# Optimization experiments

Hardware: AMD Instinct MI355X
Metric: run time of the kernel (lower is better)

## Reference

```python
import jax, jax.numpy as jnp
import numpy as np
from jax import lax

IN_CH = 64
OUT_CH = 64
K = 3
CW = 2 * IN_CH + 49  # in_ch_weight = 2*in_ch + MAX_DISPLACEMENT**2 = 177
B = 8


def setup_inputs() -> dict:
    key = jax.random.key(0)
    ks = jax.random.split(key, 14)
    f = lambda k, s, sc: jax.random.normal(k, s, dtype=jnp.float32) * sc
    he5 = lambda cin: (2.0 / (cin * 25)) ** 0.5
    he3 = lambda cin: (2.0 / (cin * 9)) ** 0.5
    return {
        "x0": f(ks[0], (B, IN_CH, 128, 160), 1.0),
        "y0": f(ks[1], (B, IN_CH, 128, 160), 1.0),
        "x": f(ks[2], (B, IN_CH, 64, 80), 1.0),
        "y": f(ks[3], (B, IN_CH, 64, 80), 1.0),
        # weight-branch 0 (outputs CW channels)
        "w1a": f(ks[4], (IN_CH, CW, 5, 5), he5(CW)),
        "w1b": f(ks[5], (IN_CH, IN_CH, 5, 5), he5(IN_CH)),
        "w1c": f(ks[6], (CW, IN_CH, 3, 3), he3(IN_CH)),
        # weight-branch 1 / final (outputs OUT_CH channels)
        "w2a": f(ks[7], (IN_CH, CW, 5, 5), he5(CW)),
        "w2b": f(ks[8], (IN_CH, IN_CH, 5, 5), he5(IN_CH)),
        "w2c": f(ks[9], (OUT_CH, IN_CH, 3, 3), he3(IN_CH)),
        # grouped 1x1 dynamic-weight generators (per-channel affine maps)
        "wx_w": f(ks[10], (CW, CW * K * K), 0.05),
        "wx_b": f(ks[11], (CW, CW * K * K), 0.05),
        "wxf_w": f(ks[12], (OUT_CH, OUT_CH * K * K), 0.05),
        "wxf_b": f(ks[13], (OUT_CH, OUT_CH * K * K), 0.05),
    }


def _conv(x, w, stride, pad):
    return lax.conv_general_dilated(
        x, w, (stride, stride), [(pad, pad), (pad, pad)],
        dimension_numbers=("NCHW", "OIHW", "NCHW"))


def _pool2(x):
    b, c, h, w = x.shape
    return x.reshape(b, c, h // 2, 2, w // 2, 2).mean(axis=(3, 5))


def _corr(x0, y0):
    # FlowNet-style correlation: max_displacement=7, stride2=2 ->
    # displacements {-6,-4,-2,0,2,4,6}^2 = 49 channels; mean over C.
    b, c, h, w = x0.shape
    D = 6
    yp = jnp.pad(y0, ((0, 0), (0, 0), (D, D), (D, D)))
    outs = []
    for dy in range(-6, 7, 2):
        for dx in range(-6, 7, 2):
            ys = yp[:, :, D + dy:D + dy + h, D + dx:D + dx + w]
            outs.append(jnp.mean(x0 * ys, axis=1))
    return jnp.stack(outs, axis=1)  # [B, 49, H, W]


def _branch(feat, wa, wb, wc):
    h = jax.nn.relu(_conv(feat, wa, 2, 2))
    h = jax.nn.relu(_conv(h, wb, 2, 2))
    h = _conv(h, wc, 2, 1)
    return h.mean(axis=(2, 3))  # adaptive_avg_pool2d -> (1,1), squeezed: [B, Cout]


def _adaptive_conv(x, w, pad):
    # per-sample conv weights w: [B, Cout, Cin, k, k]
    def one(xb, wb):
        return _conv(xb[None], wb, 1, pad)[0]
    return jax.vmap(one)(x, w)


def reference(x0, y0, x, y, w1a, w1b, w1c, w2a, w2b, w2c, wx_w, wx_b, wxf_w, wxf_b):
    b = x.shape[0]
    x0p = _pool2(x0)
    y0p = _pool2(y0)
    corr = _corr(x0p, y0p)                      # [B, 49, H, W]
    feat = jnp.concatenate([corr, x, y], axis=1)  # [B, CW, H, W]

    # iteration 0 (N-1 = 1): generate per-sample [CW,CW,3,3] filters, apply
    fv = _branch(feat, w1a, w1b, w1c)           # [B, CW]
    wx = (fv[:, :, None] * wx_w[None] + wx_b[None]).reshape(b, CW, CW, K, K)
    feat = jax.nn.relu(_adaptive_conv(feat, wx, K // 2))

    # final: generate per-sample [OUT_CH,OUT_CH,3,3] filters and return them
    fv = _branch(feat, w2a, w2b, w2c)           # [B, OUT_CH]
    wxf = (fv[:, :, None] * wxf_w[None] + wxf_b[None]).reshape(b, OUT_CH, OUT_CH, K, K)
    return wxf
```

## Files before the change

kernel.cpp:

```cpp
#include <hip/hip_runtime.h>

typedef unsigned short u16;
typedef __attribute__((ext_vector_type(8))) short bf16x8;
typedef __attribute__((ext_vector_type(4))) float f32x4;

static constexpr int B  = 8;
static constexpr int C  = 64;
static constexpr int CW = 177;
static constexpr int H  = 64, W  = 80;
static constexpr int HP = 68, WP = 84, KC = 192;
static constexpr int PB = HP * WP * KC;
static constexpr int HA = 36, WA = 44;

__device__ __forceinline__ u16 f2b(float f) {
  union { float f; unsigned u; } v; v.f = f;
  unsigned u = v.u;
  return (u16)((u + 0x7FFF + ((u >> 16) & 1)) >> 16);
}
__device__ __forceinline__ float blo(unsigned u) {
  union { unsigned v; float f; } t; t.v = u << 16; return t.f;
}
__device__ __forceinline__ float bhi(unsigned u) {
  union { unsigned v; float f; } t; t.v = u & 0xffff0000u; return t.f;
}
__device__ __forceinline__ unsigned pk2(u16 a, u16 b) {
  return (unsigned)a | ((unsigned)b << 16);
}

__global__ void zfill2(u16* __restrict__ p1, int n1, u16* __restrict__ p2, int n2) {
  int i = blockIdx.x * blockDim.x + threadIdx.x;
  bf16x8 z = 0;
  if (i < n1) ((bf16x8*)p1)[i] = z;
  else if (i < n1 + n2) ((bf16x8*)p2)[i - n1] = z;
}

__global__ __launch_bounds__(256) void pool2_kernel(const float* __restrict__ x0, const float* __restrict__ y0,
                                                    u16* __restrict__ xpT, u16* __restrict__ ypT) {
  __shared__ u16 lt[80][66];
  int blk = blockIdx.x;
  int sel = blk & 1; int h = (blk >> 1) & 63; int b = blk >> 7;
  const float* in = sel ? y0 : x0;
  u16* out = sel ? ypT : xpT;
  int tid = threadIdx.x;
#pragma unroll
  for (int i = 0; i < 20; ++i) {
    int e = i * 256 + tid;
    int c = e / 80, w = e % 80;
    const float* p = in + ((size_t)(b * 64 + c) * 128 + 2 * h) * 160 + 2 * w;
    float2 r0 = *(const float2*)p;
    float2 r1 = *(const float2*)(p + 160);
    lt[w][c] = f2b(0.25f * (r0.x + r0.y + r1.x + r1.y));
  }
  __syncthreads();
#pragma unroll
  for (int i = 0; i < 20; ++i) {
    int e = i * 256 + tid;
    int w = e / 64, c = e % 64;
    out[((size_t)(b * H + h) * W + w) * C + c] = lt[w][c];
  }
}

__global__ void corr_fill(const u16* __restrict__ xpT, const u16* __restrict__ ypT,
                          u16* __restrict__ featP) {
  int idx = blockIdx.x * blockDim.x + threadIdx.x;
  if (idx >= B * H * W * 49) return;
  int o = idx % 49; int p = idx / 49;
  int w = p % W; int h = (p / W) % H; int b = p / (W * H);
  int dy = (o / 7) * 2 - 6, dx = (o % 7) * 2 - 6;
  int hh = h + dy, ww = w + dx;
  float s = 0.f;
  if (hh >= 0 && hh < H && ww >= 0 && ww < W) {
    const uint4* xv = (const uint4*)(xpT + ((size_t)(b * H + h) * W + w) * C);
    const uint4* yv = (const uint4*)(ypT + ((size_t)(b * H + hh) * W + ww) * C);
#pragma unroll
    for (int i = 0; i < 8; ++i) {
      uint4 a = xv[i], q = yv[i];
      s += blo(a.x) * blo(q.x) + bhi(a.x) * bhi(q.x);
      s += blo(a.y) * blo(q.y) + bhi(a.y) * bhi(q.y);
      s += blo(a.z) * blo(q.z) + bhi(a.z) * bhi(q.z);
      s += blo(a.w) * blo(q.w) + bhi(a.w) * bhi(q.w);
    }
  }
  s *= (1.0f / 64.0f);
  featP[((size_t)(b * HP + h + 2) * WP + (w + 2)) * KC + o] = f2b(s);
}

__global__ __launch_bounds__(256) void copy_tr(const float* __restrict__ x, const float* __restrict__ y,
                                               u16* __restrict__ featP) {
  __shared__ float lt[40][129];
  int blk = blockIdx.x;
  int half = blk & 1; int h = (blk >> 1) & 63; int b = blk >> 7;
  int tid = threadIdx.x;
#pragma unroll
  for (int i = 0; i < 20; ++i) {
    int e = i * 256 + tid;
    int c2 = e / 40, w = e % 40;
    const float* src = (c2 < 64) ? x : y;
    int c = c2 & 63;
    lt[w][c2] = src[((size_t)(b * 64 + c) * H + h) * W + half * 40 + w];
  }
  __syncthreads();
#pragma unroll
  for (int i = 0; i < 20; ++i) {
    int e = i * 256 + tid;
    int wr = e / 128, c = e % 128;
    featP[((size_t)(b * HP + h + 2) * WP + (half * 40 + wr + 2)) * KC + 49 + c] = f2b(lt[wr][c]);
  }
}

__global__ void pack_all(const float* __restrict__ w1a, const float* __restrict__ w2a,
                         const float* __restrict__ w1b, const float* __restrict__ w2b,
                         u16* __restrict__ A5a, u16* __restrict__ A5b,
                         u16* __restrict__ A5b1, u16* __restrict__ A5b2) {
  int idx = blockIdx.x * blockDim.x + threadIdx.x;
  const int s1 = 25 * 64 * 192, s2 = 25 * 64 * 64;
  if (idx < 2 * s1) {
    const float* w = idx < s1 ? w1a : w2a; u16* A = idx < s1 ? A5a : A5b;
    int e = idx % s1;
    int j = e % 192; int i = (e / 192) % 64; int kk = e / (192 * 64);
    int ky = kk / 5, kx = kk % 5;
    float v = (j < CW) ? w[(((size_t)i * CW + j) * 5 + ky) * 5 + kx] : 0.f;
    A[e] = f2b(v);
  } else if (idx < 2 * s1 + 2 * s2) {
    int t = idx - 2 * s1;
    const float* w = t < s2 ? w1b : w2b; u16* A = t < s2 ? A5b1 : A5b2;
    int e = t % s2;
    int j = e % 64; int i = (e / 64) % 64; int kk = e / (64 * 64);
    int ky = kk / 5, kx = kk % 5;
    A[e] = f2b(w[(((size_t)i * 64 + j) * 5 + ky) * 5 + kx]);
  }
}

__global__ void halo_fill(u16* __restrict__ featP) {
  int idx = blockIdx.x * blockDim.x + threadIdx.x;
  if (idx >= B * 592 * 24) return;
  int ch = idx % 24; int pi = (idx / 24) % 592; int b = idx / (24 * 592);
  int row, col;
  if (pi < 336) {
    int r = pi / 84; row = (r < 2) ? r : r + 64; col = pi % 84;
  } else {
    int pj = pi - 336; row = 2 + (pj >> 2);
    int cc = pj & 3; col = (cc < 2) ? cc : cc + 80;
  }
  bf16x8 z = 0;
  *(bf16x8*)(featP + ((size_t)(b * HP + row) * WP + col) * KC + ch * 8) = z;
}

__global__ void wx_pack(const float* __restrict__ fv, const float* __restrict__ ww,
                        const float* __restrict__ wb, u16* __restrict__ Apk) {
  int idx = blockIdx.x * blockDim.x + threadIdx.x;
  if (idx >= 9 * 192 * 24) return;
  int j8 = idx % 24; int i = (idx / 24) % 192; int kk = idx / (24 * 192);
  float wwv[8], wbv[8];
#pragma unroll
  for (int jj = 0; jj < 8; ++jj) {
    int j = j8 * 8 + jj;
    if (i < CW && j < CW) {
      size_t o = ((size_t)i * CW + j) * 9 + kk;
      wwv[jj] = ww[o]; wbv[jj] = wb[o];
    } else { wwv[jj] = 0.f; wbv[jj] = 0.f; }
  }
  int rb = i >> 4, il = i & 15;
  int c = j8 >> 3, rem = j8 & 7, half = rem >> 2, kqq = rem & 3;
  size_t dst = (((((size_t)kk * 12 + rb) * 3 + c) * 2 + half) * 64 + kqq * 16 + il) * 8;
  for (int b = 0; b < B; ++b) {
    float f = (i < CW) ? fv[b * CW + i] : 0.f;
    u16 o[8];
#pragma unroll
    for (int jj = 0; jj < 8; ++jj) o[jj] = f2b(f * wwv[jj] + wbv[jj]);
    uint4 v; v.x = pk2(o[0], o[1]); v.y = pk2(o[2], o[3]); v.z = pk2(o[4], o[5]); v.w = pk2(o[6], o[7]);
    *(uint4*)(Apk + (size_t)b * 331776 + dst) = v;
  }
}

__global__ __launch_bounds__(256, 2) void ad_conv_kernel(
    const u16* __restrict__ Apk, const u16* __restrict__ featP, u16* __restrict__ outP) {
  __shared__ u16 lds[2][84 * 64];
  int bid = (int)(blockIdx.x % 8) * 64 + (int)(blockIdx.x / 8);
  int h = bid & 63; int b = bid >> 6;
  int tid = threadIdx.x;
  int lane = tid & 63; int wm = tid >> 6;
  int l15 = lane & 15, kq = lane >> 4;

  f32x4 acc[3][5];
#pragma unroll
  for (int i = 0; i < 3; ++i)
#pragma unroll
    for (int j = 0; j < 5; ++j) acc[i][j] = (f32x4){0.f, 0.f, 0.f, 0.f};

  const u16* fb = featP + (size_t)b * PB;
  const u16* Ab = Apk + (size_t)b * 331776 + (size_t)lane * 8;

  int i0 = tid, i1 = tid + 256, i2 = tid + 512;
  int q0 = i0 >> 3, s0 = i0 & 7;
  int q1 = i1 >> 3, s1 = i1 & 7;
  int q2 = i2 >> 3, s2 = i2 & 7;
  int w0 = (i0 * 16) ^ ((q0 & 7) << 4);
  int w1 = (i1 * 16) ^ ((q1 & 7) << 4);
  int w2 = (i2 * 16) ^ ((q2 & 7) << 4);
  bool a2 = i2 < 672;

  bf16x8 r0, r1, r2;
  {
    const u16* g = fb + ((size_t)(h + 1) * WP) * KC;
    r0 = *(const bf16x8*)(g + (size_t)q0 * KC + s0 * 8);
    r1 = *(const bf16x8*)(g + (size_t)q1 * KC + s1 * 8);
    if (a2) r2 = *(const bf16x8*)(g + (size_t)q2 * KC + s2 * 8);
    char* lw = (char*)lds[0];
    *(bf16x8*)(lw + w0) = r0;
    *(bf16x8*)(lw + w1) = r1;
    if (a2) *(bf16x8*)(lw + w2) = r2;
  }
  __syncthreads();

#pragma unroll
  for (int s = 0; s < 9; ++s) {
    const int c = s / 3, ty = s % 3;
    if (s < 8) {
      const int cn = (s + 1) / 3, tyn = (s + 1) % 3;
      const u16* g = fb + ((size_t)(h + 1 + tyn) * WP) * KC + cn * 64;
      r0 = *(const bf16x8*)(g + (size_t)q0 * KC + s0 * 8);
      r1 = *(const bf16x8*)(g + (size_t)q1 * KC + s1 * 8);
      if (a2) r2 = *(const bf16x8*)(g + (size_t)q2 * KC + s2 * 8);
    }
    const char* lb = (const char*)lds[s & 1];
#pragma unroll
    for (int tx = 0; tx < 3; ++tx) {
      const int tap = ty * 3 + tx;
#pragma unroll
      for (int half = 0; half < 2; ++half) {
        bf16x8 av[3], bv[5];
#pragma unroll
        for (int fm = 0; fm < 3; ++fm)
          av[fm] = *(const bf16x8*)(Ab + (size_t)(((tap * 12 + wm * 3 + fm) * 3 + c) * 2 + half) * 512);
#pragma unroll
        for (int fn = 0; fn < 5; ++fn) {
          int q = fn * 16 + l15 + tx + 1;
          int byte = ((q * 8 + half * 4 + kq) * 16) ^ ((q & 7) << 4);
          bv[fn] = *(const bf16x8*)(lb + byte);
        }
#pragma unroll
        for (int fm = 0; fm < 3; ++fm)
#pragma unroll
          for (int fn = 0; fn < 5; ++fn)
            acc[fm][fn] = __builtin_amdgcn_mfma_f32_16x16x32_bf16(av[fm], bv[fn], acc[fm][fn], 0, 0, 0);
      }
    }
    if (s < 8) {
      char* lw = (char*)lds[(s + 1) & 1];
      *(bf16x8*)(lw + w0) = r0;
      *(bf16x8*)(lw + w1) = r1;
      if (a2) *(bf16x8*)(lw + w2) = r2;
      __syncthreads();
    }
  }

#pragma unroll
  for (int fm = 0; fm < 3; ++fm) {
    int i0r = wm * 48 + fm * 16 + kq * 4;
#pragma unroll
    for (int fn = 0; fn < 5; ++fn) {
      int ow = fn * 16 + l15;
      u16* dst = outP + ((size_t)(b * HP + h + 2) * WP + (ow + 2)) * KC + i0r;
      uint2 pkv;
      pkv.x = pk2(f2b(fmaxf(acc[fm][fn][0], 0.f)), f2b(fmaxf(acc[fm][fn][1], 0.f)));
      pkv.y = pk2(f2b(fmaxf(acc[fm][fn][2], 0.f)), f2b(fmaxf(acc[fm][fn][3], 0.f)));
      *(uint2*)dst = pkv;
    }
  }
}

__global__ __launch_bounds__(128, 3) void conv5_split_kernel(
    const u16* __restrict__ A5, const u16* __restrict__ featP, u16* __restrict__ pa) {
  __shared__ u16 lds[2 * 84 * 32];
  char* lb = (char*)lds;
  int bid = (int)(blockIdx.x % 8) * 160 + (int)(blockIdx.x / 8);
  int rp = bid % 16; int ty = (bid / 16) % 5; int csel = (bid / 80) % 2; int b = bid / 160;
  int r0 = rp * 2;
  int kc0 = csel * 3;
  int tid = threadIdx.x;
  int lane = tid & 63; int wm = tid >> 6;
  int l15 = lane & 15, kq = lane >> 4;

  f32x4 acc[2][5];
#pragma unroll
  for (int i = 0; i < 2; ++i)
#pragma unroll
    for (int j = 0; j < 5; ++j) acc[i][j] = (f32x4){0.f, 0.f, 0.f, 0.f};

  const u16* fb = featP + (size_t)b * PB;
  int rowg0 = 2 * r0 + ty;

#pragma unroll
  for (int k = 0; k < 3; ++k) {
    int kc = kc0 + k;
    __syncthreads();
#pragma unroll
    for (int it = 0; it < 6; ++it) {
      int idx = it * 128 + tid;
      if (idx < 672) {
        int slot = idx & 3; int q = (idx >> 2) % 84; int row = idx / 336;
        bf16x8 v = *(const bf16x8*)(fb + ((size_t)(rowg0 + 2 * row) * WP + q) * KC + kc * 32 + slot * 8);
        int byte = (idx * 16) ^ ((q & 7) << 4);
        *(bf16x8*)(lb + byte) = v;
      }
    }
    __syncthreads();
#pragma unroll
    for (int tx = 0; tx < 5; ++tx) {
      bf16x8 av[2], bv[5];
#pragma unroll
      for (int fm = 0; fm < 2; ++fm)
        av[fm] = *(const bf16x8*)(A5 + ((size_t)((ty * 5 + tx) * 64 + wm * 32 + fm * 16 + l15)) * 192 + kc * 32 + kq * 8);
#pragma unroll
      for (int fn = 0; fn < 5; ++fn) {
        int p = fn * 16 + l15;
        int orow = p / 40, ocol = p % 40;
        int q = ocol * 2 + tx;
        int byte = (((orow * 84 + q) * 4 + kq) * 16) ^ ((q & 7) << 4);
        bv[fn] = *(const bf16x8*)(lb + byte);
      }
#pragma unroll
      for (int fm = 0; fm < 2; ++fm)
#pragma unroll
        for (int fn = 0; fn < 5; ++fn)
          acc[fm][fn] = __builtin_amdgcn_mfma_f32_16x16x32_bf16(av[fm], bv[fn], acc[fm][fn], 0, 0, 0);
    }
  }
  int slot10 = csel * 5 + ty;
#pragma unroll
  for (int fm = 0; fm < 2; ++fm) {
    int oc0 = wm * 32 + fm * 16 + kq * 4;
#pragma unroll
    for (int fn = 0; fn < 5; ++fn) {
      int p = fn * 16 + l15;
      int orow = r0 + p / 40, ocol = p % 40;
      u16* dst = pa + (((((size_t)slot10 * B + b) * 32 + orow) * 40 + ocol) * 64) + oc0;
      uint2 pkv;
      pkv.x = pk2(f2b(acc[fm][fn][0]), f2b(acc[fm][fn][1]));
      pkv.y = pk2(f2b(acc[fm][fn][2]), f2b(acc[fm][fn][3]));
      *(uint2*)dst = pkv;
    }
  }
}

__global__ void combine10(const u16* __restrict__ pa, u16* __restrict__ haP) {
  int idx = blockIdx.x * blockDim.x + threadIdx.x;
  if (idx >= B * 32 * 40 * 8) return;
  int c8 = idx & 7; int t = idx >> 3;
  int ocol = t % 40; t /= 40; int orow = t % 32; int b = t / 32;
  float s[8];
#pragma unroll
  for (int k = 0; k < 8; ++k) s[k] = 0.f;
#pragma unroll
  for (int sl = 0; sl < 10; ++sl) {
    const u16* p = pa + ((((size_t)sl * B + b) * 32 + orow) * 40 + ocol) * 64 + c8 * 8;
    uint4 v = *(const uint4*)p;
    s[0] += blo(v.x); s[1] += bhi(v.x); s[2] += blo(v.y); s[3] += bhi(v.y);
    s[4] += blo(v.z); s[5] += bhi(v.z); s[6] += blo(v.w); s[7] += bhi(v.w);
  }
  uint4 o;
  o.x = pk2(f2b(fmaxf(s[0], 0.f)), f2b(fmaxf(s[1], 0.f)));
  o.y = pk2(f2b(fmaxf(s[2], 0.f)), f2b(fmaxf(s[3], 0.f)));
  o.z = pk2(f2b(fmaxf(s[4], 0.f)), f2b(fmaxf(s[5], 0.f)));
  o.w = pk2(f2b(fmaxf(s[6], 0.f)), f2b(fmaxf(s[7], 0.f)));
  *(uint4*)(haP + ((size_t)(b * HA + orow + 2) * WA + (ocol + 2)) * 64 + c8 * 8) = o;
}

template<int TY, int TX, int S, int OH, int OW, int M, int BM, int BN, int POFF,
         int KCIN, int HPIN, int WPIN>
__global__ __launch_bounds__(256) void gemm_conv(
    const u16* __restrict__ A, const u16* __restrict__ featP,
    float* __restrict__ outF, int MT, int NT) {
  constexpr int WM = BM / 2, WN = BN / 2, FM = WM / 16, FN = WN / 16;
  constexpr int NKC = KCIN / 32;
  int nwg = gridDim.x;
  int bid = (int)(blockIdx.x % 8) * (nwg / 8) + (int)(blockIdx.x / 8);
  int mt = bid % MT; int rest = bid / MT; int nt = rest % NT; int b = rest / NT;
  int lane = threadIdx.x & 63; int wv = threadIdx.x >> 6;
  int wm = wv >> 1, wn = wv & 1;
  int l15 = lane & 15, kq = lane >> 4;

  f32x4 acc[FM][FN];
#pragma unroll
  for (int i = 0; i < FM; ++i)
#pragma unroll
    for (int j = 0; j < FN; ++j) acc[i][j] = (f32x4){0.f, 0.f, 0.f, 0.f};

  const u16* Abase = A + (size_t)(mt * BM + wm * WM + l15) * KCIN + kq * 8;
  const u16* fb = featP + (size_t)b * (HPIN * WPIN * KCIN) + kq * 8;

  int ohh[FN], oww[FN];
#pragma unroll
  for (int fn = 0; fn < FN; ++fn) {
    int p = nt * BN + wn * WN + fn * 16 + l15;
    ohh[fn] = p / OW; oww[fn] = p % OW;
  }

  for (int kc = 0; kc < NKC; ++kc) {
    for (int ty = 0; ty < TY; ++ty)
      for (int tx = 0; tx < TX; ++tx) {
        const u16* At = Abase + (size_t)((ty * TX + tx) * M) * KCIN + kc * 32;
        bf16x8 av[FM], bv[FN];
#pragma unroll
        for (int fm = 0; fm < FM; ++fm)
          av[fm] = *(const bf16x8*)(At + fm * 16 * KCIN);
#pragma unroll
        for (int fn = 0; fn < FN; ++fn) {
          int hi = ohh[fn] * S + ty + POFF;
          int wi = oww[fn] * S + tx + POFF;
          bv[fn] = *(const bf16x8*)(fb + (size_t)(hi * WPIN + wi) * KCIN + kc * 32);
        }
#pragma unroll
        for (int fm = 0; fm < FM; ++fm)
#pragma unroll
          for (int fn = 0; fn < FN; ++fn)
            acc[fm][fn] = __builtin_amdgcn_mfma_f32_16x16x32_bf16(av[fm], bv[fn], acc[fm][fn], 0, 0, 0);
      }
  }

#pragma unroll
  for (int fm = 0; fm < FM; ++fm) {
    int oc0 = mt * BM + wm * WM + fm * 16 + kq * 4;
#pragma unroll
    for (int fn = 0; fn < FN; ++fn) {
#pragma unroll
      for (int r = 0; r < 4; ++r) {
        float v = fmaxf(acc[fm][fn][r], 0.f);
        outF[(((size_t)b * M + oc0 + r) * OH + ohh[fn]) * OW + oww[fn]] = v;
      }
    }
  }
}

__global__ void tapsum_kernel(const float* __restrict__ hb, float* __restrict__ Sm) {
  int b = blockIdx.x >> 6; int ic = blockIdx.x & 63; int lane = threadIdx.x;
  const float* p = hb + ((size_t)(b * 64 + ic)) * 320;
  float s[9];
#pragma unroll
  for (int t = 0; t < 9; ++t) s[t] = 0.f;
  for (int i = lane; i < 320; i += 64) {
    int ih = i / 20, iw = i % 20;
    float v = p[i];
#pragma unroll
    for (int ky = 0; ky < 3; ++ky) {
      int t2 = ih + 1 - ky;
      if (t2 < 0 || t2 > 14 || (t2 & 1)) continue;
#pragma unroll
      for (int kx = 0; kx < 3; ++kx) {
        int t3 = iw + 1 - kx;
        if (t3 < 0 || t3 > 18 || (t3 & 1)) continue;
        s[ky * 3 + kx] += v;
      }
    }
  }
#pragma unroll
  for (int t = 0; t < 9; ++t)
#pragma unroll
    for (int off = 32; off > 0; off >>= 1) s[t] += __shfl_down(s[t], off);
  if (lane == 0) {
#pragma unroll
    for (int t = 0; t < 9; ++t) Sm[(b * 64 + ic) * 9 + t] = s[t];
  }
}

__global__ void gemv_fv(const float* __restrict__ w3, const float* __restrict__ Sm,
                        float* __restrict__ fv, int OC) {
  int o = blockIdx.x % OC; int b = blockIdx.x / OC; int lane = threadIdx.x;
  const float* wp = w3 + ((size_t)o * 64 + lane) * 9;
  const float* sp = Sm + ((size_t)b * 64 + lane) * 9;
  float acc = 0.f;
#pragma unroll
  for (int t = 0; t < 9; ++t) acc += wp[t] * sp[t];
#pragma unroll
  for (int off = 32; off > 0; off >>= 1) acc += __shfl_down(acc, off);
  if (lane == 0) fv[b * OC + o] = acc * (1.0f / 80.0f);
}

__global__ void final_kernel(const float* __restrict__ fv, const float* __restrict__ ww,
                             const float* __restrict__ wb, float* __restrict__ out) {
  int idx = blockIdx.x * blockDim.x + threadIdx.x;
  if (idx >= B * 64 * 576) return;
  int kk = idx % 576; int i = (idx / 576) % 64; int b = idx / (576 * 64);
  out[idx] = fv[b * 64 + i] * ww[i * 576 + kk] + wb[i * 576 + kk];
}

extern "C" void kernel_launch(void* const* d_in, const int* in_sizes, int n_in,
                              void* d_out, int out_size, void* d_ws, size_t ws_size,
                              hipStream_t stream) {
  const float* x0    = (const float*)d_in[0];
  const float* y0    = (const float*)d_in[1];
  const float* x     = (const float*)d_in[2];
  const float* y     = (const float*)d_in[3];
  const float* w1a   = (const float*)d_in[4];
  const float* w1b   = (const float*)d_in[5];
  const float* w1c   = (const float*)d_in[6];
  const float* w2a   = (const float*)d_in[7];
  const float* w2b   = (const float*)d_in[8];
  const float* w2c   = (const float*)d_in[9];
  const float* wx_w  = (const float*)d_in[10];
  const float* wx_b  = (const float*)d_in[11];
  const float* wxf_w = (const float*)d_in[12];
  const float* wxf_b = (const float*)d_in[13];
  float* out = (float*)d_out;

  char* base = (char*)d_ws;
  size_t off = 0;
  auto take = [&](size_t bytes) -> char* {
    char* p = base + off; off += (bytes + 255) & ~(size_t)255; return p;
  };
  u16*   featP1 = (u16*)take((size_t)B * PB * 2);
  u16*   featP2 = (u16*)take((size_t)B * PB * 2);
  u16*   xpT    = featP2;
  u16*   ypT    = featP2 + (size_t)B * H * W * C;
  u16*   paAwx  = (u16*)take((size_t)10 * B * 32 * 40 * 64 * 2);
  u16*   pa     = paAwx;
  u16*   Apk    = paAwx;
  u16*   A5a    = (u16*)take((size_t)25 * 64 * 192 * 2);
  u16*   A5b    = (u16*)take((size_t)25 * 64 * 192 * 2);
  u16*   A5b1   = (u16*)take((size_t)25 * 64 * 64 * 2);
  u16*   A5b2   = (u16*)take((size_t)25 * 64 * 64 * 2);
  u16*   haP    = (u16*)take((size_t)B * HA * WA * 64 * 2);
  float* hb     = (float*)take((size_t)B * 64 * 320 * 4);
  float* Sm     = (float*)take((size_t)B * 64 * 9 * 4);
  float* fv1    = (float*)take((size_t)B * CW * 4);
  float* fv2    = (float*)take((size_t)B * 64 * 4);
  if (off > ws_size) return;

  const int TB = 256;
  int nf1 = (B * PB) / 8;
  int nha = (B * HA * WA * 64) / 8;

  zfill2<<<(nf1 + nha + TB - 1) / TB, TB, 0, stream>>>(featP1, nf1, haP, nha);
  pool2_kernel<<<B * 64 * 2, TB, 0, stream>>>(x0, y0, xpT, ypT);
  {
    int n = B * H * W * 49;
    corr_fill<<<(n + TB - 1) / TB, TB, 0, stream>>>(xpT, ypT, featP1);
  }
  copy_tr<<<B * 64 * 2, TB, 0, stream>>>(x, y, featP1);
  {
    int n = 2 * 25 * 64 * 192 + 2 * 25 * 64 * 64;
    pack_all<<<(n + TB - 1) / TB, TB, 0, stream>>>(w1a, w2a, w1b, w2b, A5a, A5b, A5b1, A5b2);
  }
  halo_fill<<<(B * 592 * 24 + TB - 1) / TB, TB, 0, stream>>>(featP2);

  conv5_split_kernel<<<1280, 128, 0, stream>>>(A5a, featP1, pa);
  combine10<<<(B * 32 * 40 * 8 + TB - 1) / TB, TB, 0, stream>>>(pa, haP);
  gemm_conv<5, 5, 2, 16, 20, 64, 32, 32, 0, 64, HA, WA>
      <<<160, TB, 0, stream>>>(A5b1, haP, hb, 2, 10);
  tapsum_kernel<<<B * 64, 64, 0, stream>>>(hb, Sm);
  gemv_fv<<<B * CW, 64, 0, stream>>>(w1c, Sm, fv1, CW);

  wx_pack<<<(9 * 192 * 24 + TB - 1) / TB, TB, 0, stream>>>(fv1, wx_w, wx_b, Apk);
  ad_conv_kernel<<<64 * B, 256, 0, stream>>>(Apk, featP1, featP2);

  conv5_split_kernel<<<1280, 128, 0, stream>>>(A5b, featP2, pa);
  combine10<<<(B * 32 * 40 * 8 + TB - 1) / TB, TB, 0, stream>>>(pa, haP);
  gemm_conv<5, 5, 2, 16, 20, 64, 32, 32, 0, 64, HA, WA>
      <<<160, TB, 0, stream>>>(A5b2, haP, hb, 2, 10);
  tapsum_kernel<<<B * 64, 64, 0, stream>>>(hb, Sm);
  gemv_fv<<<B * 64, 64, 0, stream>>>(w2c, Sm, fv2, 64);

  final_kernel<<<(B * 64 * 576 + TB - 1) / TB, TB, 0, stream>>>(fv2, wxf_w, wxf_b, out);
}
```

Before: 215.8 us.

## Fuse setup kernels, double-buffer conv5 LDS, add MFMA priority, merge branch tail

Merges the zero-fill, halo-fill and weight-pack kernels into one setup launch, and fuses tapsum and gemv into a single per-batch branch_tail kernel, cutting launch count. conv5_split gets double-buffered LDS so the next channel chunk's global loads overlap the MFMA work. s_setprio is raised around MFMA blocks in conv5 and ad_conv. The pooled buffers move to the paAwx scratch region, and branch_tail runs only 8 blocks, which may underuse the GPU.

```diff
diff --git a/kernel.cpp b/kernel.cpp
--- a/kernel.cpp
+++ b/kernel.cpp
@@ -27,11 +27,48 @@
   return (unsigned)a | ((unsigned)b << 16);
 }
 
-__global__ void zfill2(u16* __restrict__ p1, int n1, u16* __restrict__ p2, int n2) {
-  int i = blockIdx.x * blockDim.x + threadIdx.x;
+__global__ void setup_kernel(
+    const float* __restrict__ w1a, const float* __restrict__ w2a,
+    const float* __restrict__ w1b, const float* __restrict__ w2b,
+    u16* __restrict__ A5a, u16* __restrict__ A5b,
+    u16* __restrict__ A5b1, u16* __restrict__ A5b2,
+    u16* __restrict__ featP1, u16* __restrict__ haP, u16* __restrict__ featP2) {
+  int idx = blockIdx.x * blockDim.x + threadIdx.x;
+  const int n0r = (B * PB) / 8;
+  const int n1r = (B * HA * WA * 64) / 8;
+  const int n2r = B * 592 * 24;
+  const int s1 = 25 * 64 * 192, s2 = 25 * 64 * 64;
   bf16x8 z = 0;
-  if (i < n1) ((bf16x8*)p1)[i] = z;
-  else if (i < n1 + n2) ((bf16x8*)p2)[i - n1] = z;
+  if (idx < n0r) { ((bf16x8*)featP1)[idx] = z; return; }
+  idx -= n0r;
+  if (idx < n1r) { ((bf16x8*)haP)[idx] = z; return; }
+  idx -= n1r;
+  if (idx < n2r) {
+    int ch = idx % 24; int pi = (idx / 24) % 592; int b = idx / (24 * 592);
+    int row, col;
+    if (pi < 336) { int rr = pi / 84; row = (rr < 2) ? rr : rr + 64; col = pi % 84; }
+    else { int pj = pi - 336; row = 2 + (pj >> 2); int cc = pj & 3; col = (cc < 2) ? cc : cc + 80; }
+    *(bf16x8*)(featP2 + ((size_t)(b * HP + row) * WP + col) * KC + ch * 8) = z;
+    return;
+  }
+  idx -= n2r;
+  if (idx < 2 * s1) {
+    const float* w = idx < s1 ? w1a : w2a; u16* A = idx < s1 ? A5a : A5b;
+    int e = idx % s1;
+    int j = e % 192; int i = (e / 192) % 64; int kk = e / (192 * 64);
+    int ky = kk / 5, kx = kk % 5;
+    float v = (j < CW) ? w[(((size_t)i * CW + j) * 5 + ky) * 5 + kx] : 0.f;
+    A[e] = f2b(v);
+    return;
+  }
+  idx -= 2 * s1;
+  if (idx < 2 * s2) {
+    const float* w = idx < s2 ? w1b : w2b; u16* A = idx < s2 ? A5b1 : A5b2;
+    int e = idx % s2;
+    int j = e % 64; int i = (e / 64) % 64; int kk = e / (64 * 64);
+    int ky = kk / 5, kx = kk % 5;
+    A[e] = f2b(w[(((size_t)i * 64 + j) * 5 + ky) * 5 + kx]);
+  }
 }
 
 __global__ __launch_bounds__(256) void pool2_kernel(const float* __restrict__ x0, const float* __restrict__ y0,
@@ -108,44 +145,6 @@
   }
 }
 
-__global__ void pack_all(const float* __restrict__ w1a, const float* __restrict__ w2a,
-                         const float* __restrict__ w1b, const float* __restrict__ w2b,
-                         u16* __restrict__ A5a, u16* __restrict__ A5b,
-                         u16* __restrict__ A5b1, u16* __restrict__ A5b2) {
-  int idx = blockIdx.x * blockDim.x + threadIdx.x;
-  const int s1 = 25 * 64 * 192, s2 = 25 * 64 * 64;
-  if (idx < 2 * s1) {
-    const float* w = idx < s1 ? w1a : w2a; u16* A = idx < s1 ? A5a : A5b;
-    int e = idx % s1;
-    int j = e % 192; int i = (e / 192) % 64; int kk = e / (192 * 64);
-    int ky = kk / 5, kx = kk % 5;
-    float v = (j < CW) ? w[(((size_t)i * CW + j) * 5 + ky) * 5 + kx] : 0.f;
-    A[e] = f2b(v);
-  } else if (idx < 2 * s1 + 2 * s2) {
-    int t = idx - 2 * s1;
-    const float* w = t < s2 ? w1b : w2b; u16* A = t < s2 ? A5b1 : A5b2;
-    int e = t % s2;
-    int j = e % 64; int i = (e / 64) % 64; int kk = e / (64 * 64);
-    int ky = kk / 5, kx = kk % 5;
-    A[e] = f2b(w[(((size_t)i * 64 + j) * 5 + ky) * 5 + kx]);
-  }
-}
-
-__global__ void halo_fill(u16* __restrict__ featP) {
-  int idx = blockIdx.x * blockDim.x + threadIdx.x;
-  if (idx >= B * 592 * 24) return;
-  int ch = idx % 24; int pi = (idx / 24) % 592; int b = idx / (24 * 592);
-  int row, col;
-  if (pi < 336) {
-    int r = pi / 84; row = (r < 2) ? r : r + 64; col = pi % 84;
-  } else {
-    int pj = pi - 336; row = 2 + (pj >> 2);
-    int cc = pj & 3; col = (cc < 2) ? cc : cc + 80;
-  }
-  bf16x8 z = 0;
-  *(bf16x8*)(featP + ((size_t)(b * HP + row) * WP + col) * KC + ch * 8) = z;
-}
-
 __global__ void wx_pack(const float* __restrict__ fv, const float* __restrict__ ww,
                         const float* __restrict__ wb, u16* __restrict__ Apk) {
   int idx = blockIdx.x * blockDim.x + threadIdx.x;
@@ -228,22 +227,24 @@
     for (int tx = 0; tx < 3; ++tx) {
       const int tap = ty * 3 + tx;
 #pragma unroll
-      for (int half = 0; half < 2; ++half) {
+      for (int hk = 0; hk < 2; ++hk) {
         bf16x8 av[3], bv[5];
 #pragma unroll
         for (int fm = 0; fm < 3; ++fm)
-          av[fm] = *(const bf16x8*)(Ab + (size_t)(((tap * 12 + wm * 3 + fm) * 3 + c) * 2 + half) * 512);
+          av[fm] = *(const bf16x8*)(Ab + (size_t)(((tap * 12 + wm * 3 + fm) * 3 + c) * 2 + hk) * 512);
 #pragma unroll
         for (int fn = 0; fn < 5; ++fn) {
           int q = fn * 16 + l15 + tx + 1;
-          int byte = ((q * 8 + half * 4 + kq) * 16) ^ ((q & 7) << 4);
+          int byte = ((q * 8 + hk * 4 + kq) * 16) ^ ((q & 7) << 4);
           bv[fn] = *(const bf16x8*)(lb + byte);
         }
+        __builtin_amdgcn_s_setprio(1);
 #pragma unroll
         for (int fm = 0; fm < 3; ++fm)
 #pragma unroll
           for (int fn = 0; fn < 5; ++fn)
             acc[fm][fn] = __builtin_amdgcn_mfma_f32_16x16x32_bf16(av[fm], bv[fn], acc[fm][fn], 0, 0, 0);
+        __builtin_amdgcn_s_setprio(0);
       }
     }
     if (s < 8) {
@@ -272,8 +273,7 @@
 
 __global__ __launch_bounds__(128, 3) void conv5_split_kernel(
     const u16* __restrict__ A5, const u16* __restrict__ featP, u16* __restrict__ pa) {
-  __shared__ u16 lds[2 * 84 * 32];
-  char* lb = (char*)lds;
+  __shared__ u16 lds[2][84 * 64];
   int bid = (int)(blockIdx.x % 8) * 160 + (int)(blockIdx.x / 8);
   int rp = bid % 16; int ty = (bid / 16) % 5; int csel = (bid / 80) % 2; int b = bid / 160;
   int r0 = rp * 2;
@@ -291,21 +291,39 @@
   const u16* fb = featP + (size_t)b * PB;
   int rowg0 = 2 * r0 + ty;
 
-#pragma unroll
-  for (int k = 0; k < 3; ++k) {
-    int kc = kc0 + k;
-    __syncthreads();
+  bf16x8 r[6];
+  auto load_chunk = [&](int kc) {
 #pragma unroll
     for (int it = 0; it < 6; ++it) {
       int idx = it * 128 + tid;
       if (idx < 672) {
         int slot = idx & 3; int q = (idx >> 2) % 84; int row = idx / 336;
-        bf16x8 v = *(const bf16x8*)(fb + ((size_t)(rowg0 + 2 * row) * WP + q) * KC + kc * 32 + slot * 8);
+        r[it] = *(const bf16x8*)(fb + ((size_t)(rowg0 + 2 * row) * WP + q) * KC + kc * 32 + slot * 8);
+      }
+    }
+  };
+  auto write_chunk = [&](int buf) {
+    char* lw = (char*)lds[buf];
+#pragma unroll
+    for (int it = 0; it < 6; ++it) {
+      int idx = it * 128 + tid;
+      if (idx < 672) {
+        int q = (idx >> 2) % 84;
         int byte = (idx * 16) ^ ((q & 7) << 4);
-        *(bf16x8*)(lb + byte) = v;
-      }
-    }
-    __syncthreads();
+        *(bf16x8*)(lw + byte) = r[it];
+      }
+    }
+  };
+
+  load_chunk(kc0);
+  write_chunk(0);
+  __syncthreads();
+
+#pragma unroll
+  for (int k = 0; k < 3; ++k) {
+    int kc = kc0 + k;
+    if (k < 2) load_chunk(kc + 1);
+    const char* lb = (const char*)lds[k & 1];
 #pragma unroll
     for (int tx = 0; tx < 5; ++tx) {
       bf16x8 av[2], bv[5];
@@ -320,11 +338,17 @@
         int byte = (((orow * 84 + q) * 4 + kq) * 16) ^ ((q & 7) << 4);
         bv[fn] = *(const bf16x8*)(lb + byte);
       }
+      __builtin_amdgcn_s_setprio(1);
 #pragma unroll
       for (int fm = 0; fm < 2; ++fm)
 #pragma unroll
         for (int fn = 0; fn < 5; ++fn)
           acc[fm][fn] = __builtin_amdgcn_mfma_f32_16x16x32_bf16(av[fm], bv[fn], acc[fm][fn], 0, 0, 0);
+      __builtin_amdgcn_s_setprio(0);
+    }
+    if (k < 2) {
+      write_chunk((k + 1) & 1);
+      __syncthreads();
     }
   }
   int slot10 = csel * 5 + ty;
@@ -433,15 +457,22 @@
   }
 }
 
-__global__ void tapsum_kernel(const float* __restrict__ hb, float* __restrict__ Sm) {
-  int b = blockIdx.x >> 6; int ic = blockIdx.x & 63; int lane = threadIdx.x;
-  const float* p = hb + ((size_t)(b * 64 + ic)) * 320;
+__global__ __launch_bounds__(256) void branch_tail(
+    const float* __restrict__ hb, const float* __restrict__ w3,
+    float* __restrict__ fv, int OC) {
+  __shared__ float sp[4][64][9];
+  __shared__ float Sl[64][9];
+  int b = blockIdx.x;
+  int tid = threadIdx.x;
+  int ic = tid & 63, grp = tid >> 6;
   float s[9];
 #pragma unroll
   for (int t = 0; t < 9; ++t) s[t] = 0.f;
-  for (int i = lane; i < 320; i += 64) {
+  const float* p = hb + ((size_t)(b * 64 + ic)) * 320 + grp * 80;
+  for (int j = 0; j < 80; ++j) {
+    int i = grp * 80 + j;
     int ih = i / 20, iw = i % 20;
-    float v = p[i];
+    float v = p[j];
 #pragma unroll
     for (int ky = 0; ky < 3; ++ky) {
       int t2 = ih + 1 - ky;
@@ -455,26 +486,26 @@
     }
   }
 #pragma unroll
-  for (int t = 0; t < 9; ++t)
-#pragma unroll
-    for (int off = 32; off > 0; off >>= 1) s[t] += __shfl_down(s[t], off);
-  if (lane == 0) {
-#pragma unroll
-    for (int t = 0; t < 9; ++t) Sm[(b * 64 + ic) * 9 + t] = s[t];
-  }
-}
-
-__global__ void gemv_fv(const float* __restrict__ w3, const float* __restrict__ Sm,
-                        float* __restrict__ fv, int OC) {
-  int o = blockIdx.x % OC; int b = blockIdx.x / OC; int lane = threadIdx.x;
-  const float* wp = w3 + ((size_t)o * 64 + lane) * 9;
-  const float* sp = Sm + ((size_t)b * 64 + lane) * 9;
-  float acc = 0.f;
-#pragma unroll
-  for (int t = 0; t < 9; ++t) acc += wp[t] * sp[t];
-#pragma unroll
-  for (int off = 32; off > 0; off >>= 1) acc += __shfl_down(acc, off);
-  if (lane == 0) fv[b * OC + o] = acc * (1.0f / 80.0f);
+  for (int t = 0; t < 9; ++t) sp[grp][ic][t] = s[t];
+  __syncthreads();
+  for (int e = tid; e < 576; e += 256) {
+    int ic2 = e / 9, t2 = e % 9;
+    Sl[ic2][t2] = sp[0][ic2][t2] + sp[1][ic2][t2] + sp[2][ic2][t2] + sp[3][ic2][t2];
+  }
+  __syncthreads();
+  if (tid < OC) {
+    const float* wp = w3 + (size_t)tid * 576;
+    float a0 = 0.f, a1 = 0.f, a2 = 0.f;
+    for (int ic2 = 0; ic2 < 64; ++ic2) {
+#pragma unroll
+      for (int t = 0; t < 9; t += 3) {
+        a0 += wp[ic2 * 9 + t]     * Sl[ic2][t];
+        a1 += wp[ic2 * 9 + t + 1] * Sl[ic2][t + 1];
+        a2 += wp[ic2 * 9 + t + 2] * Sl[ic2][t + 2];
+      }
+    }
+    fv[b * OC + tid] = (a0 + a1 + a2) * (1.0f / 80.0f);
+  }
 }
 
 __global__ void final_kernel(const float* __restrict__ fv, const float* __restrict__ ww,
@@ -511,45 +542,41 @@
   };
   u16*   featP1 = (u16*)take((size_t)B * PB * 2);
   u16*   featP2 = (u16*)take((size_t)B * PB * 2);
-  u16*   xpT    = featP2;
-  u16*   ypT    = featP2 + (size_t)B * H * W * C;
   u16*   paAwx  = (u16*)take((size_t)10 * B * 32 * 40 * 64 * 2);
   u16*   pa     = paAwx;
   u16*   Apk    = paAwx;
+  u16*   xpT    = paAwx;
+  u16*   ypT    = paAwx + (size_t)B * H * W * C;
   u16*   A5a    = (u16*)take((size_t)25 * 64 * 192 * 2);
   u16*   A5b    = (u16*)take((size_t)25 * 64 * 192 * 2);
   u16*   A5b1   = (u16*)take((size_t)25 * 64 * 64 * 2);
   u16*   A5b2   = (u16*)take((size_t)25 * 64 * 64 * 2);
   u16*   haP    = (u16*)take((size_t)B * HA * WA * 64 * 2);
   float* hb     = (float*)take((size_t)B * 64 * 320 * 4);
-  float* Sm     = (float*)take((size_t)B * 64 * 9 * 4);
   float* fv1    = (float*)take((size_t)B * CW * 4);
   float* fv2    = (float*)take((size_t)B * 64 * 4);
   if (off > ws_size) return;
 
   const int TB = 256;
-  int nf1 = (B * PB) / 8;
-  int nha = (B * HA * WA * 64) / 8;
-
-  zfill2<<<(nf1 + nha + TB - 1) / TB, TB, 0, stream>>>(featP1, nf1, haP, nha);
+
+  {
+    int n = (B * PB) / 8 + (B * HA * WA * 64) / 8 + B * 592 * 24
+          + 2 * 25 * 64 * 192 + 2 * 25 * 64 * 64;
+    setup_kernel<<<(n + TB - 1) / TB, TB, 0, stream>>>(
+        w1a, w2a, w1b, w2b, A5a, A5b, A5b1, A5b2, featP1, haP, featP2);
+  }
   pool2_kernel<<<B * 64 * 2, TB, 0, stream>>>(x0, y0, xpT, ypT);
   {
     int n = B * H * W * 49;
     corr_fill<<<(n + TB - 1) / TB, TB, 0, stream>>>(xpT, ypT, featP1);
   }
   copy_tr<<<B * 64 * 2, TB, 0, stream>>>(x, y, featP1);
-  {
-    int n = 2 * 25 * 64 * 192 + 2 * 25 * 64 * 64;
-    pack_all<<<(n + TB - 1) / TB, TB, 0, stream>>>(w1a, w2a, w1b, w2b, A5a, A5b, A5b1, A5b2);
-  }
-  halo_fill<<<(B * 592 * 24 + TB - 1) / TB, TB, 0, stream>>>(featP2);
 
   conv5_split_kernel<<<1280, 128, 0, stream>>>(A5a, featP1, pa);
   combine10<<<(B * 32 * 40 * 8 + TB - 1) / TB, TB, 0, stream>>>(pa, haP);
   gemm_conv<5, 5, 2, 16, 20, 64, 32, 32, 0, 64, HA, WA>
       <<<160, TB, 0, stream>>>(A5b1, haP, hb, 2, 10);
-  tapsum_kernel<<<B * 64, 64, 0, stream>>>(hb, Sm);
-  gemv_fv<<<B * CW, 64, 0, stream>>>(w1c, Sm, fv1, CW);
+  branch_tail<<<B, TB, 0, stream>>>(hb, w1c, fv1, CW);
 
   wx_pack<<<(9 * 192 * 24 + TB - 1) / TB, TB, 0, stream>>>(fv1, wx_w, wx_b, Apk);
   ad_conv_kernel<<<64 * B, 256, 0, stream>>>(Apk, featP1, featP2);
@@ -558,8 +585,7 @@
   combine10<<<(B * 32 * 40 * 8 + TB - 1) / TB, TB, 0, stream>>>(pa, haP);
   gemm_conv<5, 5, 2, 16, 20, 64, 32, 32, 0, 64, HA, WA>
       <<<160, TB, 0, stream>>>(A5b2, haP, hb, 2, 10);
-  tapsum_kernel<<<B * 64, 64, 0, stream>>>(hb, Sm);
-  gemv_fv<<<B * 64, 64, 0, stream>>>(w2c, Sm, fv2, 64);
+  branch_tail<<<B, TB, 0, stream>>>(hb, w2c, fv2, 64);
 
   final_kernel<<<(B * 64 * 576 + TB - 1) / TB, TB, 0, stream>>>(fv2, wxf_w, wxf_b, out);
 }
```

After: 253.5 us. 1.17x slower.
